# Performance work log

Hardware: AMD Instinct MI355X
Metric: run time of the kernel (lower is better)

The kernel has to match this reference:

```python
import jax, jax.numpy as jnp
import numpy as np

D_MODEL = 512
NHEAD = 8
HEAD_DIM = D_MODEL // NHEAD
D_FF = 2048
EPS = 1e-5


def _linear_params(key, d_in, d_out):
    kw, kb = jax.random.split(key)
    bound = 1.0 / np.sqrt(d_in)
    W = jax.random.uniform(kw, (d_out, d_in), jnp.float32, -bound, bound)
    b = jax.random.uniform(kb, (d_out,), jnp.float32, -bound, bound)
    return W, b


def setup_inputs() -> dict:
    key = jax.random.key(0)
    ks = jax.random.split(key, 8)
    src = jax.random.normal(ks[0], (4, 2048, D_MODEL), jnp.float32)
    Wq, bq = _linear_params(ks[1], D_MODEL, D_MODEL)
    Wk, bk = _linear_params(ks[2], D_MODEL, D_MODEL)
    Wv, bv = _linear_params(ks[3], D_MODEL, D_MODEL)
    Wo, bo = _linear_params(ks[4], D_MODEL, D_MODEL)
    W1, b1 = _linear_params(ks[5], D_MODEL, D_FF)
    W2, b2 = _linear_params(ks[6], D_FF, D_MODEL)
    g1 = jnp.ones((D_MODEL,), jnp.float32)
    be1 = jnp.zeros((D_MODEL,), jnp.float32)
    g2 = jnp.ones((D_MODEL,), jnp.float32)
    be2 = jnp.zeros((D_MODEL,), jnp.float32)
    return dict(src=src, Wq=Wq, bq=bq, Wk=Wk, bk=bk, Wv=Wv, bv=bv,
                Wo=Wo, bo=bo, W1=W1, b1=b1, W2=W2, b2=b2,
                g1=g1, be1=be1, g2=g2, be2=be2)


def _layer_norm(x, g, b):
    mu = jnp.mean(x, axis=-1, keepdims=True)
    var = jnp.mean(jnp.square(x - mu), axis=-1, keepdims=True)
    return (x - mu) / jnp.sqrt(var + EPS) * g + b


def reference(src, Wq, bq, Wk, bk, Wv, bv, Wo, bo, W1, b1, W2, b2, g1, be1, g2, be2):
    B, T, D = src.shape
    scale = np.sqrt(HEAD_DIM).astype(np.float32)
    # Projections (torch Linear: x @ W.T + b)
    Q = (src @ Wq.T + bq).reshape(B, T, NHEAD, HEAD_DIM).transpose(0, 2, 1, 3)
    K = (src @ Wk.T + bk).reshape(B, T, NHEAD, HEAD_DIM).transpose(0, 2, 1, 3)
    V = (src @ Wv.T + bv).reshape(B, T, NHEAD, HEAD_DIM).transpose(0, 2, 1, 3)
    # Explicit QK^T -> softmax -> V (no mask, dropout=0)
    scores = jnp.einsum('bhqd,bhkd->bhqk', Q, K) / scale  # (B,H,T,T)
    attn = jax.nn.softmax(scores, axis=-1)
    ctx = jnp.einsum('bhqk,bhkd->bhqd', attn, V)
    ctx = ctx.transpose(0, 2, 1, 3).reshape(B, T, D)
    attn_out = ctx @ Wo.T + bo
    # Add & Norm 1
    x = _layer_norm(src + attn_out, g1, be1)
    # FFN: Linear -> GELU -> Linear
    h = jax.nn.gelu(x @ W1.T + b1, approximate=False)
    ffn_out = h @ W2.T + b2
    # Add & Norm 2
    return _layer_norm(x + ffn_out, g2, be2)
```

## Files before the change

### kernel.cpp

```cpp
#include <hip/hip_runtime.h>
#include <hip/hip_bf16.h>
#include <hip/hip_fp16.h>
#include <math.h>

typedef __bf16 bf16_t;
typedef __bf16 bf16x8 __attribute__((ext_vector_type(8)));
typedef __bf16 bf16x2 __attribute__((ext_vector_type(2)));
typedef float  f32x4  __attribute__((ext_vector_type(4)));

#define D_MODEL 512
#define NHEAD   8
#define HD      64
#define D_FF    2048
#define TOKENS  8192
#define SEQ     2048
#define BATCH   4

__device__ __forceinline__ void gload16(const bf16_t* g, bf16_t* l)
{
    __builtin_amdgcn_global_load_lds(
        (const __attribute__((address_space(1))) void*)g,
        (__attribute__((address_space(3))) void*)l,
        16, 0, 0);
}

__device__ __forceinline__ void cvt4(const float* s, bf16_t* d)
{
    float4 v = *(const float4*)s;
    alignas(8) bf16_t t[4] = {(bf16_t)v.x, (bf16_t)v.y, (bf16_t)v.z, (bf16_t)v.w};
    *(uint2*)d = *(const uint2*)t;
}

__global__ void cvt_weights(const float* __restrict__ src,
                            const float* __restrict__ Wq, const float* __restrict__ Wk,
                            const float* __restrict__ Wv, const float* __restrict__ Wo,
                            const float* __restrict__ W1, const float* __restrict__ W2,
                            const float* __restrict__ bq, const float* __restrict__ bk,
                            const float* __restrict__ bv,
                            bf16_t* __restrict__ Xb,
                            bf16_t* __restrict__ Wqkvb, bf16_t* __restrict__ Wob,
                            bf16_t* __restrict__ W1b, bf16_t* __restrict__ W2b,
                            float* __restrict__ bqkv, float* __restrict__ zbias)
{
    int i = blockIdx.x * 256 + threadIdx.x;
    if (i < 1048576) { cvt4(src + (size_t)i * 4, Xb + (size_t)i * 4); return; }
    i -= 1048576;
    if (i < 65536)        cvt4(Wq + (size_t)i * 4,            Wqkvb + (size_t)i * 4);
    else if (i < 131072)  cvt4(Wk + (size_t)(i - 65536) * 4,  Wqkvb + (size_t)i * 4);
    else if (i < 196608)  cvt4(Wv + (size_t)(i - 131072) * 4, Wqkvb + (size_t)i * 4);
    else if (i < 262144)  cvt4(Wo + (size_t)(i - 196608) * 4, Wob + (size_t)(i - 196608) * 4);
    else if (i < 524288)  cvt4(W1 + (size_t)(i - 262144) * 4, W1b + (size_t)(i - 262144) * 4);
    else if (i < 786432)  cvt4(W2 + (size_t)(i - 524288) * 4, W2b + (size_t)(i - 524288) * 4);
    else if (i < 786816) {
        int j = i - 786432;
        const float* s = (j < 128) ? bq + j * 4 : (j < 256) ? bk + (j - 128) * 4
                                                            : bv + (j - 256) * 4;
        *(float4*)(bqkv + (j & 127) * 4 + (j >> 7) * 512) = *(const float4*)s;
    } else if (i < 786944) {
        int j = i - 786816;
        *(float4*)(zbias + j * 4) = make_float4(0.f, 0.f, 0.f, 0.f);
    }
}

template <int BM, int EPI, bool SPLIT2>
__global__ __launch_bounds__(256)
void gemm_bt(const bf16_t* __restrict__ A, const bf16_t* __restrict__ B,
             const float* __restrict__ bias, const float* __restrict__ biasz,
             void* __restrict__ Cout, int M, int N, int K)
{
    constexpr int MI = BM / 32;
    __shared__ bf16_t sA[2][BM][32];
    __shared__ bf16_t sB[2][128][32];
    bf16_t* sAf = &sA[0][0][0];
    bf16_t* sBf = &sB[0][0][0];

    const int tid  = threadIdx.x;
    const int wave = tid >> 6;
    const int lane = tid & 63;
    const int g    = lane >> 4;
    const int c16  = lane & 15;
    const int wm   = (wave >> 1) * (BM / 2);
    const int wn   = (wave & 1) * 64;
    const int m0   = blockIdx.y * BM;
    const int n0   = blockIdx.x * 128;

    const int zz    = SPLIT2 ? blockIdx.z : 0;
    const int Keff  = SPLIT2 ? (K >> 1) : K;
    const int kbase = zz * Keff;
    const float* bptr = (SPLIT2 && zz) ? biasz : bias;

    const f32x4 fz = {0.f, 0.f, 0.f, 0.f};
    f32x4 acc[MI][4];
#pragma unroll
    for (int i = 0; i < MI; i++)
#pragma unroll
        for (int j = 0; j < 4; j++) acc[i][j] = fz;

    const int srow = tid >> 2;
    const int scol = (tid & 3) * 8;
    const bf16_t* pa = A + (size_t)(m0 + srow) * K + kbase + scol;
    const bf16_t* pb = B + (size_t)(n0 + srow) * K + kbase + scol;

#pragma unroll
    for (int i = 0; i < BM / 64; i++)
        gload16(pa + (size_t)i * 64 * K, sAf + i * 2048 + tid * 8);
#pragma unroll
    for (int i = 0; i < 2; i++)
        gload16(pb + (size_t)i * 64 * K, sBf + i * 2048 + tid * 8);

    const int NK = Keff >> 5;
    for (int kk = 0; kk < NK; ++kk) {
        const int cur = kk & 1;
        __syncthreads();
        if (kk + 1 < NK) {
            const int k0 = (kk + 1) * 32;
            bf16_t* dA = sAf + (cur ^ 1) * (BM * 32);
            bf16_t* dB = sBf + (cur ^ 1) * 4096;
#pragma unroll
            for (int i = 0; i < BM / 64; i++)
                gload16(pa + (size_t)i * 64 * K + k0, dA + i * 2048 + tid * 8);
#pragma unroll
            for (int i = 0; i < 2; i++)
                gload16(pb + (size_t)i * 64 * K + k0, dB + i * 2048 + tid * 8);
        }

        bf16x8 af[MI], bfr[4];
#pragma unroll
        for (int i = 0; i < MI; i++)
            af[i] = *(const bf16x8*)&sA[cur][wm + i * 16 + c16][g * 8];
#pragma unroll
        for (int j = 0; j < 4; j++)
            bfr[j] = *(const bf16x8*)&sB[cur][wn + j * 16 + c16][g * 8];
#pragma unroll
        for (int mi = 0; mi < MI; mi++)
#pragma unroll
            for (int ni = 0; ni < 4; ni++)
                acc[mi][ni] = __builtin_amdgcn_mfma_f32_16x16x32_bf16(
                    af[mi], bfr[ni], acc[mi][ni], 0, 0, 0);
    }

    __half* outh = (__half*)Cout + (size_t)zz * M * N;
#pragma unroll
    for (int mi = 0; mi < MI; mi++) {
#pragma unroll
        for (int ni = 0; ni < 4; ni++) {
            const int col = n0 + wn + ni * 16 + c16;
            const float bv = bptr[col];
#pragma unroll
            for (int r = 0; r < 4; r++) {
                const int row = m0 + wm + mi * 16 + g * 4 + r;
                float v = acc[mi][ni][r] + bv;
                if (EPI == 1) v = 0.5f * v * (1.f + erff(v * 0.70710678118654752f));
                if (EPI == 2)
                    outh[(size_t)row * N + col] = (__half)v;
                else
                    ((bf16_t*)Cout)[(size_t)row * N + col] = (bf16_t)v;
            }
        }
    }
}

__global__ __launch_bounds__(256)
void transpose_v(const bf16_t* __restrict__ qkv, bf16_t* __restrict__ vt)
{
    __shared__ bf16_t st[64][72];
    const int t0 = blockIdx.x * 64;
    const int bh = blockIdx.y;
    const int b = bh >> 3, h = bh & 7;
    const int tid = threadIdx.x;

    for (int c = tid; c < 512; c += 256) {
        int r = c >> 3, cj = (c & 7) * 8;
        const bf16_t* src = qkv + ((size_t)(b * SEQ + t0 + r)) * 1536 + 1024 + h * 64 + cj;
        *(int4*)&st[r][cj] = *(const int4*)src;
    }
    __syncthreads();
    for (int c = tid; c < 512; c += 256) {
        int d = c >> 3, pj = (c & 7) * 8;
        alignas(16) bf16_t tmp[8];
#pragma unroll
        for (int j = 0; j < 8; j++) {
            int p = pj + j;
            int t = ((p >> 5) << 5) + (((p >> 2) & 1) << 4) + (((p >> 3) & 3) << 2) + (p & 3);
            tmp[j] = st[t][d];
        }
        *(int4*)(vt + ((size_t)(bh * 64 + d)) * SEQ + t0 + pj) = *(const int4*)tmp;
    }
}

__global__ __launch_bounds__(256)
__attribute__((amdgpu_waves_per_eu(2, 2)))
void flash_attn(const bf16_t* __restrict__ qkv, const bf16_t* __restrict__ vt,
                bf16_t* __restrict__ ctx)
{
    __shared__ bf16_t sK[2][64][64];
    __shared__ bf16_t sVt[2][64][64];

    const int bh = blockIdx.y;
    const int b = bh >> 3, h = bh & 7;
    const int q0 = blockIdx.x * 128;
    const int tid = threadIdx.x;
    const int wave = tid >> 6, lane = tid & 63;
    const int g = lane >> 4, c16 = lane & 15;

    const float qscale = 0.125f * 1.4426950408889634f;
    bf16x8 aq[2][2];
#pragma unroll
    for (int qt = 0; qt < 2; qt++)
#pragma unroll
        for (int ks = 0; ks < 2; ks++) {
            bf16x8 v = *(const bf16x8*)(qkv +
                ((size_t)(b * SEQ + q0 + wave * 32 + qt * 16 + c16)) * 1536 +
                h * 64 + ks * 32 + g * 8);
#pragma unroll
            for (int j = 0; j < 8; j++) v[j] = (bf16_t)((float)v[j] * qscale);
            aq[qt][ks] = v;
        }

    const f32x4 fz = {0.f, 0.f, 0.f, 0.f};
    f32x4 acc_oT[4][2];
#pragma unroll
    for (int dt = 0; dt < 4; dt++)
#pragma unroll
        for (int qt = 0; qt < 2; qt++) acc_oT[dt][qt] = fz;
    float l_acc[2] = {0.f, 0.f};

    const int f0 = tid,        r0 = f0 >> 3, l0 = (f0 & 7) ^ (r0 & 7);
    const int f1 = tid + 256,  r1 = f1 >> 3, l1 = (f1 & 7) ^ (r1 & 7);
    const bf16_t* gK0 = qkv + ((size_t)(b * SEQ + r0)) * 1536 + 512 + h * 64 + l0 * 8;
    const bf16_t* gK1 = qkv + ((size_t)(b * SEQ + r1)) * 1536 + 512 + h * 64 + l1 * 8;
    const bf16_t* gV0 = vt + ((size_t)(bh * 64 + r0)) * SEQ + l0 * 8;
    const bf16_t* gV1 = vt + ((size_t)(bh * 64 + r1)) * SEQ + l1 * 8;
    bf16_t* lK = &sK[0][0][0];
    bf16_t* lV = &sVt[0][0][0];

    gload16(gK0, lK + f0 * 8);
    gload16(gK1, lK + f1 * 8);
    gload16(gV0, lV + f0 * 8);
    gload16(gV1, lV + f1 * 8);

    for (int it = 0; it < 32; ++it) {
        const int cur = it & 1;
        __syncthreads();
        if (it < 31) {
            const size_t kv = (size_t)(it + 1) * 64;
            const int bo = (cur ^ 1) * 4096;
            gload16(gK0 + kv * 1536, lK + bo + f0 * 8);
            gload16(gK1 + kv * 1536, lK + bo + f1 * 8);
            gload16(gV0 + kv,        lV + bo + f0 * 8);
            gload16(gV1 + kv,        lV + bo + f1 * 8);
        }

        f32x4 accs[4][2];
#pragma unroll
        for (int tt = 0; tt < 4; tt++)
#pragma unroll
            for (int qt = 0; qt < 2; qt++) accs[tt][qt] = fz;
#pragma unroll
        for (int ks = 0; ks < 2; ks++) {
            const int pc = ((ks * 4 + g) ^ (c16 & 7)) * 8;
#pragma unroll
            for (int tt = 0; tt < 4; tt++) {
                bf16x8 ak = *(const bf16x8*)&sK[cur][tt * 16 + c16][pc];
                accs[tt][0] = __builtin_amdgcn_mfma_f32_16x16x32_bf16(ak, aq[0][ks], accs[tt][0], 0, 0, 0);
                accs[tt][1] = __builtin_amdgcn_mfma_f32_16x16x32_bf16(ak, aq[1][ks], accs[tt][1], 0, 0, 0);
            }
        }

#pragma unroll
        for (int tt = 0; tt < 4; tt++)
#pragma unroll
            for (int qt = 0; qt < 2; qt++) {
                float s = 0.f;
#pragma unroll
                for (int r = 0; r < 4; r++) {
                    float p = __builtin_amdgcn_exp2f(accs[tt][qt][r]);
                    accs[tt][qt][r] = p;
                    s += p;
                }
                l_acc[qt] += s;
            }
        bf16x8 pb[2][2];
#pragma unroll
        for (int qt = 0; qt < 2; qt++)
#pragma unroll
            for (int kv = 0; kv < 2; kv++)
#pragma unroll
                for (int j = 0; j < 8; j++)
                    pb[qt][kv][j] = (bf16_t)accs[kv * 2 + (j >> 2)][qt][j & 3];

#pragma unroll
        for (int kv = 0; kv < 2; kv++) {
            const int pc = ((kv * 4 + g) ^ (c16 & 7)) * 8;
#pragma unroll
            for (int dt = 0; dt < 4; dt++) {
                bf16x8 av = *(const bf16x8*)&sVt[cur][dt * 16 + c16][pc];
                acc_oT[dt][0] = __builtin_amdgcn_mfma_f32_16x16x32_bf16(av, pb[0][kv], acc_oT[dt][0], 0, 0, 0);
                acc_oT[dt][1] = __builtin_amdgcn_mfma_f32_16x16x32_bf16(av, pb[1][kv], acc_oT[dt][1], 0, 0, 0);
            }
        }
    }

#pragma unroll
    for (int qt = 0; qt < 2; qt++) {
        float l = l_acc[qt];
        l += __shfl_xor(l, 16);
        l += __shfl_xor(l, 32);
        const float inv = 1.0f / l;
        const int token = q0 + wave * 32 + qt * 16 + c16;
        bf16_t* dst = ctx + ((size_t)(b * SEQ + token)) * 512 + h * 64 + g * 4;
#pragma unroll
        for (int dt = 0; dt < 4; dt++) {
            alignas(8) bf16_t o4[4];
#pragma unroll
            for (int r = 0; r < 4; r++) o4[r] = (bf16_t)(acc_oT[dt][qt][r] * inv);
            *(uint2*)(dst + dt * 16) = *(const uint2*)o4;
        }
    }
}

__global__ __launch_bounds__(256)
void add_ln3(const float* __restrict__ a, const __half* __restrict__ b,
             const __half* __restrict__ c,
             const float* __restrict__ gamma, const float* __restrict__ beta,
             float* __restrict__ outf, bf16_t* __restrict__ outb)
{
    const int row  = blockIdx.x * 4 + (threadIdx.x >> 6);
    const int lane = threadIdx.x & 63;
    const size_t base = (size_t)row * 512 + lane * 8;

    int4 braw = *(const int4*)(b + base);
    int4 craw = *(const int4*)(c + base);
    const __half* bh = (const __half*)&braw;
    const __half* ch = (const __half*)&craw;

    float v[8];
#pragma unroll
    for (int hh = 0; hh < 2; hh++) {
        float4 av = *(const float4*)(a + base + hh * 4);
        v[hh * 4 + 0] = av.x + (float)bh[hh * 4 + 0] + (float)ch[hh * 4 + 0];
        v[hh * 4 + 1] = av.y + (float)bh[hh * 4 + 1] + (float)ch[hh * 4 + 1];
        v[hh * 4 + 2] = av.z + (float)bh[hh * 4 + 2] + (float)ch[hh * 4 + 2];
        v[hh * 4 + 3] = av.w + (float)bh[hh * 4 + 3] + (float)ch[hh * 4 + 3];
    }

    float s = 0.f;
#pragma unroll
    for (int i = 0; i < 8; i++) s += v[i];
#pragma unroll
    for (int off = 32; off > 0; off >>= 1) s += __shfl_xor(s, off);
    const float mu = s * (1.f / 512.f);

    float q = 0.f;
#pragma unroll
    for (int i = 0; i < 8; i++) { float d = v[i] - mu; q += d * d; }
#pragma unroll
    for (int off = 32; off > 0; off >>= 1) q += __shfl_xor(q, off);
    const float rstd = rsqrtf(q * (1.f / 512.f) + 1e-5f);

    float4 g0 = *(const float4*)(gamma + lane * 8);
    float4 g1 = *(const float4*)(gamma + lane * 8 + 4);
    float4 e0 = *(const float4*)(beta + lane * 8);
    float4 e1 = *(const float4*)(beta + lane * 8 + 4);
    const float gg[8] = {g0.x, g0.y, g0.z, g0.w, g1.x, g1.y, g1.z, g1.w};
    const float ee[8] = {e0.x, e0.y, e0.z, e0.w, e1.x, e1.y, e1.z, e1.w};

    float o[8];
#pragma unroll
    for (int i = 0; i < 8; i++) o[i] = (v[i] - mu) * rstd * gg[i] + ee[i];

    *(float4*)(outf + base)     = make_float4(o[0], o[1], o[2], o[3]);
    *(float4*)(outf + base + 4) = make_float4(o[4], o[5], o[6], o[7]);
    if (outb) {
        alignas(16) bf16_t ob[8];
#pragma unroll
        for (int i = 0; i < 8; i++) ob[i] = (bf16_t)o[i];
        *(int4*)(outb + base) = *(const int4*)ob;
    }
}

extern "C" void kernel_launch(void* const* d_in, const int* in_sizes, int n_in,
                              void* d_out, int out_size, void* d_ws, size_t ws_size,
                              hipStream_t stream)
{
    const float* src = (const float*)d_in[0];
    const float* Wq  = (const float*)d_in[1];  const float* bq  = (const float*)d_in[2];
    const float* Wk  = (const float*)d_in[3];  const float* bk  = (const float*)d_in[4];
    const float* Wv  = (const float*)d_in[5];  const float* bv  = (const float*)d_in[6];
    const float* Wo  = (const float*)d_in[7];  const float* bo  = (const float*)d_in[8];
    const float* W1  = (const float*)d_in[9];  const float* b1  = (const float*)d_in[10];
    const float* W2  = (const float*)d_in[11]; const float* b2  = (const float*)d_in[12];
    const float* g1  = (const float*)d_in[13]; const float* be1 = (const float*)d_in[14];
    const float* g2  = (const float*)d_in[15]; const float* be2 = (const float*)d_in[16];
    float* out = (float*)d_out;

    char* ws = (char*)d_ws;
    size_t off = 0;
    auto alloc = [&](size_t bytes) -> void* {
        void* p = ws + off;
        off = (off + bytes + 255) & ~(size_t)255;
        return p;
    };

    bf16_t* Xb    = (bf16_t*)alloc((size_t)TOKENS * 512 * 2);
    bf16_t* Wqkvb = (bf16_t*)alloc((size_t)1536 * 512 * 2);
    bf16_t* Wob   = (bf16_t*)alloc((size_t)512 * 512 * 2);
    bf16_t* W1b   = (bf16_t*)alloc((size_t)2048 * 512 * 2);
    bf16_t* W2b   = (bf16_t*)alloc((size_t)512 * 2048 * 2);
    float*  bqkv  = (float*)alloc(1536 * 4);
    float*  zbias = (float*)alloc(512 * 4);
    bf16_t* QKV   = (bf16_t*)alloc((size_t)TOKENS * 1536 * 2);
    bf16_t* Vt    = (bf16_t*)alloc((size_t)32 * 64 * SEQ * 2);
    bf16_t* CTX   = (bf16_t*)alloc((size_t)TOKENS * 512 * 2);
    __half* ATTa  = (__half*)alloc((size_t)TOKENS * 512 * 2);
    __half* ATTb  = (__half*)alloc((size_t)TOKENS * 512 * 2);
    float*  X1    = (float*)alloc((size_t)TOKENS * 512 * 4);
    bf16_t* X1b   = (bf16_t*)alloc((size_t)TOKENS * 512 * 2);

    bf16_t* H    = QKV;
    __half* FFNa = ATTa;
    __half* FFNb = ATTb;

    cvt_weights<<<7170, 256, 0, stream>>>(src, Wq, Wk, Wv, Wo, W1, W2, bq, bk, bv,
                                          Xb, Wqkvb, Wob, W1b, W2b, bqkv, zbias);

    gemm_bt<128, 0, false><<<dim3(12, 64), 256, 0, stream>>>(
        Xb, Wqkvb, bqkv, zbias, QKV, TOKENS, 1536, 512);

    transpose_v<<<dim3(32, 32), 256, 0, stream>>>(QKV, Vt);
    flash_attn<<<dim3(16, 32), 256, 0, stream>>>(QKV, Vt, CTX);

    gemm_bt<64, 2, true><<<dim3(4, 128, 2), 256, 0, stream>>>(
        CTX, Wob, bo, zbias, ATTa, TOKENS, 512, 512);

    add_ln3<<<2048, 256, 0, stream>>>(src, ATTa, ATTb, g1, be1, X1, X1b);

    gemm_bt<128, 1, false><<<dim3(16, 64), 256, 0, stream>>>(
        X1b, W1b, b1, zbias, H, TOKENS, 2048, 512);

    gemm_bt<64, 2, true><<<dim3(4, 128, 2), 256, 0, stream>>>(
        H, W2b, b2, zbias, FFNa, TOKENS, 512, 2048);

    add_ln3<<<2048, 256, 0, stream>>>(X1, FFNa, FFNb, g2, be2, out, nullptr);
}
```

Before: 281.3 us.

## Double GEMM K-step to 64 and XOR-swizzle LDS layout

The bf16 GEMM now stages 64-wide K slices per pipeline stage instead of 32, halving the number of barriers and load rounds per tile. The LDS layout applies an XOR swizzle on the 16-byte chunk index keyed by row, so the MFMA fragment reads avoid bank conflicts with the wider 128-byte row stride. The cost is doubled shared memory per block, which may lower occupancy, and it requires K/2 to be a multiple of 64 on the split path.

New measurement: 279.2 us. No clear change (-0.7%).

```diff
diff --git a/kernel.cpp b/kernel.cpp
--- a/kernel.cpp
+++ b/kernel.cpp
@@ -69,8 +69,9 @@
              void* __restrict__ Cout, int M, int N, int K)
 {
     constexpr int MI = BM / 32;
-    __shared__ bf16_t sA[2][BM][32];
-    __shared__ bf16_t sB[2][128][32];
+    constexpr int NA = BM / 32;
+    __shared__ bf16_t sA[2][BM][64];
+    __shared__ bf16_t sB[2][128][64];
     bf16_t* sAf = &sA[0][0][0];
     bf16_t* sBf = &sB[0][0][0];
 
@@ -96,47 +97,57 @@
 #pragma unroll
         for (int j = 0; j < 4; j++) acc[i][j] = fz;
 
-    const int srow = tid >> 2;
-    const int scol = (tid & 3) * 8;
-    const bf16_t* pa = A + (size_t)(m0 + srow) * K + kbase + scol;
-    const bf16_t* pb = B + (size_t)(n0 + srow) * K + kbase + scol;
-
-#pragma unroll
-    for (int i = 0; i < BM / 64; i++)
-        gload16(pa + (size_t)i * 64 * K, sAf + i * 2048 + tid * 8);
-#pragma unroll
-    for (int i = 0; i < 2; i++)
-        gload16(pb + (size_t)i * 64 * K, sBf + i * 2048 + tid * 8);
-
-    const int NK = Keff >> 5;
-    for (int kk = 0; kk < NK; ++kk) {
-        const int cur = kk & 1;
+    const bf16_t* gA[NA]; int fa[NA];
+#pragma unroll
+    for (int i = 0; i < NA; i++) {
+        const int f = i * 256 + tid, row = f >> 3, l = (f & 7) ^ (row & 7);
+        fa[i] = f;
+        gA[i] = A + (size_t)(m0 + row) * K + kbase + l * 8;
+    }
+    const bf16_t* gB[4]; int fb[4];
+#pragma unroll
+    for (int i = 0; i < 4; i++) {
+        const int f = i * 256 + tid, row = f >> 3, l = (f & 7) ^ (row & 7);
+        fb[i] = f;
+        gB[i] = B + (size_t)(n0 + row) * K + kbase + l * 8;
+    }
+
+#pragma unroll
+    for (int i = 0; i < NA; i++) gload16(gA[i], sAf + fa[i] * 8);
+#pragma unroll
+    for (int i = 0; i < 4; i++)  gload16(gB[i], sBf + fb[i] * 8);
+
+    const int NS = Keff >> 6;
+    for (int s = 0; s < NS; ++s) {
+        const int cur = s & 1;
         __syncthreads();
-        if (kk + 1 < NK) {
-            const int k0 = (kk + 1) * 32;
-            bf16_t* dA = sAf + (cur ^ 1) * (BM * 32);
-            bf16_t* dB = sBf + (cur ^ 1) * 4096;
-#pragma unroll
-            for (int i = 0; i < BM / 64; i++)
-                gload16(pa + (size_t)i * 64 * K + k0, dA + i * 2048 + tid * 8);
-#pragma unroll
-            for (int i = 0; i < 2; i++)
-                gload16(pb + (size_t)i * 64 * K + k0, dB + i * 2048 + tid * 8);
-        }
-
-        bf16x8 af[MI], bfr[4];
-#pragma unroll
-        for (int i = 0; i < MI; i++)
-            af[i] = *(const bf16x8*)&sA[cur][wm + i * 16 + c16][g * 8];
-#pragma unroll
-        for (int j = 0; j < 4; j++)
-            bfr[j] = *(const bf16x8*)&sB[cur][wn + j * 16 + c16][g * 8];
-#pragma unroll
-        for (int mi = 0; mi < MI; mi++)
-#pragma unroll
-            for (int ni = 0; ni < 4; ni++)
-                acc[mi][ni] = __builtin_amdgcn_mfma_f32_16x16x32_bf16(
-                    af[mi], bfr[ni], acc[mi][ni], 0, 0, 0);
+        if (s + 1 < NS) {
+            const int ko = (s + 1) * 64;
+            bf16_t* dA = sAf + (cur ^ 1) * (BM * 64);
+            bf16_t* dB = sBf + (cur ^ 1) * 8192;
+#pragma unroll
+            for (int i = 0; i < NA; i++) gload16(gA[i] + ko, dA + fa[i] * 8);
+#pragma unroll
+            for (int i = 0; i < 4; i++)  gload16(gB[i] + ko, dB + fb[i] * 8);
+        }
+
+#pragma unroll
+        for (int sub = 0; sub < 2; ++sub) {
+            const int ck = (((sub * 4 + g) ^ (c16 & 7))) * 8;
+            bf16x8 af[MI], bfr[4];
+#pragma unroll
+            for (int i = 0; i < MI; i++)
+                af[i] = *(const bf16x8*)&sA[cur][wm + i * 16 + c16][ck];
+#pragma unroll
+            for (int j = 0; j < 4; j++)
+                bfr[j] = *(const bf16x8*)&sB[cur][wn + j * 16 + c16][ck];
+#pragma unroll
+            for (int mi = 0; mi < MI; mi++)
+#pragma unroll
+                for (int ni = 0; ni < 4; ni++)
+                    acc[mi][ni] = __builtin_amdgcn_mfma_f32_16x16x32_bf16(
+                        af[mi], bfr[ni], acc[mi][ni], 0, 0, 0);
+        }
     }
 
     __half* outh = (__half*)Cout + (size_t)zz * M * N;
```
